# Kernel optimization log

Hardware: AMD Instinct MI355X
Metric: run time of the kernel (lower is better)

The kernel has to match this reference:

```python
import jax, jax.numpy as jnp
import numpy as np

B, L, H, NH, NE, M = 4, 1024, 768, 12, 42, 8
EMB = 768
OFFSET = 1  # bert cls offset


def setup_inputs() -> dict:
    key = jax.random.key(0)
    ks = jax.random.split(key, 6)
    seq = jax.random.normal(ks[0], (B, L, H), jnp.float32)
    attn = jax.random.uniform(ks[1], (B, NH, L, L), jnp.float32)
    attn = attn / attn.sum(-1, keepdims=True)  # row-stochastic like softmaxed attention probs
    W_head = jax.random.normal(ks[2], (2 * H, EMB), jnp.float32) * 0.02
    b_head = jnp.zeros((EMB,), jnp.float32)
    W_tail = jax.random.normal(ks[3], (2 * H, EMB), jnp.float32) * 0.02
    b_tail = jnp.zeros((EMB,), jnp.float32)
    # mention start positions (before +offset); keep start+offset < L
    mention_pos = jax.random.randint(ks[4], (B, NE, M), 0, L - OFFSET - 1)
    counts = jax.random.randint(ks[5], (B, NE), 1, M + 1)  # >=1 valid mention per entity
    mention_mask = jnp.arange(M)[None, None, :] < counts[:, :, None]
    return dict(sequence_output=seq, attention=attn, W_head=W_head, b_head=b_head,
                W_tail=W_tail, b_tail=b_tail, mention_pos=mention_pos,
                mention_mask=mention_mask)


def _get_hrt(seq, attn, mention_pos, mention_mask):
    # seq: [B,L,H]; attn: [B,NH,L,L]; mention_pos/mask: [B,NE,M]
    b_idx = jnp.arange(B)[:, None, None]
    pos = mention_pos + OFFSET                          # [B,NE,M]
    m_emb = seq[b_idx, pos]                             # [B,NE,M,H] mention embeddings
    att_t = jnp.transpose(attn, (0, 2, 1, 3))           # [B,L,NH,L]
    m_att = att_t[b_idx, pos]                           # [B,NE,M,NH,L] mention attentions
    mask = mention_mask
    neg_inf = jnp.finfo(seq.dtype).min
    # per-entity logsumexp pooling over mentions
    ent_emb = jax.nn.logsumexp(jnp.where(mask[..., None], m_emb, neg_inf), axis=2)
    has_m = mask.any(axis=2)
    ent_emb = jnp.where(has_m[..., None], ent_emb, 0.0)  # [B,NE,H]
    cnt = mask.sum(axis=2).astype(seq.dtype)
    ent_att = (m_att * mask[..., None, None].astype(seq.dtype)).sum(axis=2)
    ent_att = ent_att / jnp.maximum(cnt, 1.0)[..., None, None]  # [B,NE,NH,L] mean over mentions
    # all ordered (head, tail) pairs on the NE x NE grid
    hs = jnp.broadcast_to(ent_emb[:, :, None, :], (B, NE, NE, H))
    ts = jnp.broadcast_to(ent_emb[:, None, :, :], (B, NE, NE, H))
    # ht_att = relu(mean_h(h_att * t_att)), normalized over seq, then context = ht_att @ seq
    ht = jnp.einsum('bihl,bjhl->bijl', ent_att, ent_att) / NH  # [B,NE,NE,L]
    ht = jax.nn.relu(ht)
    ht = ht / (ht.sum(-1, keepdims=True) + 1e-10)
    rs = jnp.einsum('bijl,bld->bijd', ht, seq)                  # [B,NE,NE,H]
    return hs, rs, ts


def reference(sequence_output, attention, W_head, b_head, W_tail, b_tail, mention_pos, mention_mask):
    hs, rs, ts = _get_hrt(sequence_output, attention, mention_pos, mention_mask)
    h_out = jnp.tanh(jnp.concatenate([hs, rs], axis=-1) @ W_head + b_head)
    t_out = jnp.tanh(jnp.concatenate([ts, rs], axis=-1) @ W_tail + b_tail)
    return h_out, t_out
```

## Files before the change

### kernel.cpp

```cpp
#include <hip/hip_runtime.h>
#include <math.h>

typedef _Float16 f16;
typedef __attribute__((ext_vector_type(4))) _Float16 f16x4;
typedef __attribute__((ext_vector_type(8))) _Float16 f16x8;
typedef __attribute__((ext_vector_type(4))) float f32x4;

#define B_    4
#define L_    1024
#define H_    768
#define NH_   12
#define NE_   42
#define M_    8
#define E2_   1536
#define HTP_  1792
#define OUT_HALF 5419008LL

typedef __attribute__((address_space(1))) const unsigned char ga_t;
typedef __attribute__((address_space(3))) unsigned char la_t;
__device__ __forceinline__ void async16(const void* g, void* l) {
    __builtin_amdgcn_global_load_lds((ga_t*)g, (la_t*)l, 16, 0, 0);
}


__device__ void prep_body(int bid, char* smem,
                          const float* __restrict__ Wh, const float* __restrict__ Wt,
                          const float* __restrict__ bh, const float* __restrict__ bt,
                          f16* __restrict__ wtop, f16* __restrict__ wbot,
                          float* __restrict__ bcat) {
    float (*tile)[33] = (float(*)[33])smem;
    int tx = bid % 24, ty = (bid / 24) % 24, m = bid / 576;
    const float* src = (m & 1) ? Wt : Wh;
    int roff = (m & 2) ? H_ : 0;
    f16* dst = (m & 2) ? wbot : wtop;
    int coff = (m & 1) ? H_ : 0;
    int x = threadIdx.x & 31, y8 = threadIdx.x >> 5;
#pragma unroll
    for (int r = 0; r < 4; r++) {
        int h = ty*32 + y8 + r*8, c = tx*32 + x;
        tile[y8 + r*8][x] = src[(long long)(roff + h)*H_ + c];
    }
    __syncthreads();
#pragma unroll
    for (int r = 0; r < 4; r++) {
        int c2 = tx*32 + y8 + r*8, h2 = ty*32 + x;
        dst[(long long)(coff + c2)*H_ + h2] = (f16)tile[x][y8 + r*8];
    }
    if (bid == 0) {
        for (int idx = threadIdx.x; idx < E2_; idx += 256)
            bcat[idx] = (idx < H_) ? bh[idx] : bt[idx - H_];
    }
}

__device__ void seq16_body(int bid, const float* __restrict__ seq,
                           f16* __restrict__ seq16) {
    int idx = (bid*256 + threadIdx.x) * 4;
    f32x4 v = *(const f32x4*)(seq + idx);
    f16x4 o = {(f16)v[0], (f16)v[1], (f16)v[2], (f16)v[3]};
    *(f16x4*)(seq16 + idx) = o;
}

__device__ void ent_emb_body(int bid, const float* __restrict__ seq,
                             const int* __restrict__ mpos,
                             const int* __restrict__ mmask,
                             f16* __restrict__ ent) {
    int e = bid % NE_, b = bid / NE_;
    int tid = threadIdx.x;
    const int* mp = mpos  + (b*NE_ + e)*M_;
    const int* mk = mmask + (b*NE_ + e)*M_;
    int pos[M_], msk[M_];
#pragma unroll
    for (int m = 0; m < M_; m++) { msk[m] = mk[m]; pos[m] = mp[m] + 1; }
#pragma unroll
    for (int q = 0; q < 3; q++) {
        int h = tid + q*256;
        float mx = -1e30f, vals[M_];
#pragma unroll
        for (int m = 0; m < M_; m++) {
            vals[m] = 0.f;
            if (msk[m]) {
                float v = seq[((long long)b*L_ + pos[m])*H_ + h];
                vals[m] = v; mx = fmaxf(mx, v);
            }
        }
        float s = 0.f;
#pragma unroll
        for (int m = 0; m < M_; m++) if (msk[m]) s += expf(vals[m] - mx);
        float lse = (mx > -1e29f) ? mx + logf(s) : 0.f;
        ent[(b*NE_ + e)*H_ + h] = (f16)lse;
    }
}

__device__ void ent_att_body(int bid, const float* __restrict__ attn,
                             const int* __restrict__ mpos,
                             const int* __restrict__ mmask,
                             f16* __restrict__ eatt) {
    int nh = bid % NH_, e = (bid / NH_) % NE_, b = bid / (NH_*NE_);
    int tid = threadIdx.x;
    int l0 = tid * 4;
    const int* mp = mpos  + (b*NE_ + e)*M_;
    const int* mk = mmask + (b*NE_ + e)*M_;
    const float* abase = attn + (long long)(b*NH_ + nh) * L_ * L_;
    f32x4 acc = {0,0,0,0}; int cnt = 0;
#pragma unroll
    for (int m = 0; m < M_; m++) {
        if (mk[m]) {
            cnt++;
            const float* row = abase + (long long)(mp[m] + 1) * L_;
            acc += *(const f32x4*)(row + l0);
        }
    }
    float inv = 1.f / (float)(cnt > 0 ? cnt : 1);
    f16x4 o = {(f16)(acc[0]*inv), (f16)(acc[1]*inv), (f16)(acc[2]*inv), (f16)(acc[3]*inv)};
    *(f16x4*)(eatt + ((long long)(b*NE_ + e)*NH_ + nh)*L_ + l0) = o;
}

__device__ void ht_body(int bid, char* smem, const f16* __restrict__ eatt,
                        f16* __restrict__ HT) {
    int jg = bid % 6, i = (bid / 6) % NE_, b = bid / 252;
    int tid = threadIdx.x;
    f16* ei_s = (f16*)smem;
    float* red = (float*)(smem + NH_*L_*2);
    const f16* ei = eatt + (long long)(b*NE_ + i)*NH_*L_;
#pragma unroll
    for (int q = 0; q < 6; q++) {
        int off = (q*256 + tid)*8;
        *(f16x8*)(ei_s + off) = *(const f16x8*)(ei + off);
    }
    __syncthreads();
    int l0 = tid*4;
    int wave = tid >> 6, lane = tid & 63;
    for (int jj = 0; jj < 7; jj++) {
        int j = jg*7 + jj;
        const f16* ej = eatt + (long long)(b*NE_ + j)*NH_*L_;
        f32x4 acc = {0,0,0,0};
#pragma unroll
        for (int h = 0; h < NH_; h++) {
            f16x4 vi = *(const f16x4*)(ei_s + h*L_ + l0);
            f16x4 vj = *(const f16x4*)(ej   + h*L_ + l0);
#pragma unroll
            for (int r = 0; r < 4; r++) acc[r] += (float)vi[r] * (float)vj[r];
        }
        float v[4]; float s = 0.f;
#pragma unroll
        for (int r = 0; r < 4; r++) {
            float t = acc[r] * (1.f/12.f);
            t = t > 0.f ? t : 0.f;
            v[r] = t; s += t;
        }
#pragma unroll
        for (int m = 1; m < 64; m <<= 1) s += __shfl_xor(s, m, 64);
        if (lane == 0) red[wave] = s;
        __syncthreads();
        float S = red[0] + red[1] + red[2] + red[3];
        __syncthreads();
        float sc = 1.f / (S + 1e-10f);
        f16x4 o = {(f16)(v[0]*sc), (f16)(v[1]*sc), (f16)(v[2]*sc), (f16)(v[3]*sc)};
        *(f16x4*)(HT + ((long long)b*HTP_ + i*NE_ + j)*L_ + l0) = o;
    }
}

#define LDSS 40
__device__ void gemm_het_body(int bx, int by, char* smem,
                              const f16* __restrict__ A, const f16* __restrict__ BT,
                              float* __restrict__ het, const float* __restrict__ bcat) {
    const int M = 168, K = 768;
    f16* As = (f16*)smem;
    f16* Bs = (f16*)(smem + 64*LDSS*2);
    int bm = bx*64, bn = by*64;
    int tid = threadIdx.x;
    int wave = tid >> 6, lane = tid & 63;
    int wm = (wave >> 1)*32, wn = (wave & 1)*32;
    int lo4 = lane & 15, kq = (lane >> 4)*8;
    int srow = tid >> 2, scol = (tid & 3)*8;
    bool aval = (bm + srow) < M;
    const f16* aptr = A + (long long)(bm + srow)*K + scol;
    const f16* bptr = BT + (long long)(bn + srow)*K + scol;
    f32x4 acc[2][2] = {};
    for (int k0 = 0; k0 < K; k0 += 32) {
        uint4 zero = {0,0,0,0};
        uint4 av = aval ? *(const uint4*)(aptr + k0) : zero;
        uint4 bv = *(const uint4*)(bptr + k0);
        __syncthreads();
        *(uint4*)(As + srow*LDSS + scol) = av;
        *(uint4*)(Bs + srow*LDSS + scol) = bv;
        __syncthreads();
        f16x8 a0 = *(const f16x8*)(As + (wm +      lo4)*LDSS + kq);
        f16x8 a1 = *(const f16x8*)(As + (wm + 16 + lo4)*LDSS + kq);
        f16x8 b0 = *(const f16x8*)(Bs + (wn +      lo4)*LDSS + kq);
        f16x8 b1 = *(const f16x8*)(Bs + (wn + 16 + lo4)*LDSS + kq);
        acc[0][0] = __builtin_amdgcn_mfma_f32_16x16x32_f16(a0, b0, acc[0][0], 0,0,0);
        acc[0][1] = __builtin_amdgcn_mfma_f32_16x16x32_f16(a0, b1, acc[0][1], 0,0,0);
        acc[1][0] = __builtin_amdgcn_mfma_f32_16x16x32_f16(a1, b0, acc[1][0], 0,0,0);
        acc[1][1] = __builtin_amdgcn_mfma_f32_16x16x32_f16(a1, b1, acc[1][1], 0,0,0);
    }
    int rloc = (lane >> 4)*4;
#pragma unroll
    for (int sm = 0; sm < 2; sm++)
#pragma unroll
    for (int sn = 0; sn < 2; sn++) {
        f32x4 a = acc[sm][sn];
        int c  = bn + wn + sn*16 + lo4;
        int rb = bm + wm + sm*16 + rloc;
#pragma unroll
        for (int r = 0; r < 4; r++)
            if (rb + r < M) het[(rb + r)*E2_ + c] = a[r] + bcat[c];
    }
}

template<int MODE>
__device__ void gemm2_body(int bx, int by, int bz, char* smem,
                           const f16* __restrict__ A, const f16* __restrict__ BT, int K,
                           long long strideA, long long strideBT,
                           const float* __restrict__ het, float* __restrict__ outp,
                           f16* __restrict__ outp16) {
    f16* As = (f16*)smem;
    f16* Bs = (f16*)(smem + 8192);
    int bm = bx*128, bn = by*128;
    const f16* Ab = A + strideA*bz;
    const f16* Bb = BT + strideBT*bz;
    int tid = threadIdx.x, wave = tid >> 6, lane = tid & 63;
    int wm = (wave >> 1)*64, wn = (wave & 1)*64;
    int lo4 = lane & 15, kq = (lane >> 4)*8;
    int lrow = lane >> 2, lcol = (lane & 3)*8;
    const f16* ag = Ab + (long long)(bm + wave*32 + lrow)*K + lcol;
    const f16* bg = Bb + (long long)(bn + wave*32 + lrow)*K + lcol;
    f16* asl = As + wave*1024;
    f16* bsl = Bs + wave*1024;
    f32x4 acc[4][4] = {};
    for (int k0 = 0; k0 < K; k0 += 32) {
        async16(ag + k0,          asl);
        async16(ag + k0 + 16*K,   asl + 512);
        async16(bg + k0,          bsl);
        async16(bg + k0 + 16*K,   bsl + 512);
        __syncthreads();
        f16x8 af[4], bf[4];
#pragma unroll
        for (int s = 0; s < 4; s++) {
            af[s] = *(const f16x8*)(As + (wm + s*16 + lo4)*32 + kq);
            bf[s] = *(const f16x8*)(Bs + (wn + s*16 + lo4)*32 + kq);
        }
#pragma unroll
        for (int sm = 0; sm < 4; sm++)
#pragma unroll
        for (int sn = 0; sn < 4; sn++)
            acc[sm][sn] = __builtin_amdgcn_mfma_f32_16x16x32_f16(af[sm], bf[sn], acc[sm][sn], 0,0,0);
        __syncthreads();
    }
    int rloc = (lane >> 4)*4;
#pragma unroll
    for (int sm = 0; sm < 4; sm++)
#pragma unroll
    for (int sn = 0; sn < 4; sn++) {
        f32x4 a = acc[sm][sn];
        int c  = bn + wn + sn*16 + lo4;
        int rb = bm + wm + sm*16 + rloc;
        if constexpr (MODE == 1) {
            f16x4 o = {(f16)a[0], (f16)a[1], (f16)a[2], (f16)a[3]};
            *(f16x4*)(outp16 + (long long)bz*E2_*L_ + (long long)c*L_ + rb) = o;
        } else {
#pragma unroll
            for (int r = 0; r < 4; r++) {
                int row = rb + r;
                if (row < NE_*NE_) {
                    int i = row / NE_;
                    int j = row - i*NE_;
                    int sel = (c < H_) ? i : j;
                    float bias = het[(bz*NE_ + sel)*E2_ + c];
                    float v = tanhf(a[r] + bias);
                    long long o = (c < H_)
                        ? ((long long)((bz*NE_ + i)*NE_ + j))*H_ + c
                        : OUT_HALF + ((long long)((bz*NE_ + i)*NE_ + j))*H_ + (c - H_);
                    outp[o] = v;
                }
            }
        }
    }
}

__global__ __launch_bounds__(256) void k_L1(
        const float* __restrict__ seq, const float* __restrict__ attn,
        const float* __restrict__ Wh, const float* __restrict__ bh,
        const float* __restrict__ Wt, const float* __restrict__ bt,
        const int* __restrict__ mpos, const int* __restrict__ mmask,
        f16* __restrict__ wtop, f16* __restrict__ wbot, float* __restrict__ bcat,
        f16* __restrict__ seq16, f16* __restrict__ ent, f16* __restrict__ eatt) {
    __shared__ __align__(16) char smem[4224];
    int bid = blockIdx.x;
    if (bid < 2304)       prep_body(bid, smem, Wh, Wt, bh, bt, wtop, wbot, bcat);
    else if (bid < 5376)  seq16_body(bid - 2304, seq, seq16);
    else if (bid < 5544)  ent_emb_body(bid - 5376, seq, mpos, mmask, ent);
    else                  ent_att_body(bid - 5544, attn, mpos, mmask, eatt);
}

__global__ __launch_bounds__(256) void k_L2(
        const f16* __restrict__ seq16, const f16* __restrict__ wbot,
        const f16* __restrict__ ent, const f16* __restrict__ wtop,
        const float* __restrict__ bcat, const f16* __restrict__ eatt,
        f16* __restrict__ seqWT, float* __restrict__ het, f16* __restrict__ HT) {
    __shared__ __align__(16) char smem[24640];
    int bid = blockIdx.x;
    if (bid < 384) {
        int bx = bid & 7, by = (bid >> 3) % 12, bz = bid / 96;
        gemm2_body<1>(bx, by, bz, smem, seq16, wbot, 768,
                      (long long)L_*H_, 0, nullptr, nullptr, seqWT);
    } else if (bid < 1392) {
        ht_body(bid - 384, smem, eatt, HT);
    } else {
        int r = bid - 1392;
        gemm_het_body(r % 3, r / 3, smem, ent, wtop, het, bcat);
    }
}

__global__ __launch_bounds__(256) void k_L3(
        const f16* __restrict__ HT, const f16* __restrict__ seqWT,
        const float* __restrict__ het, float* __restrict__ outp) {
    __shared__ __align__(16) char smem[16384];
    gemm2_body<2>(blockIdx.x, blockIdx.y, blockIdx.z, smem, HT, seqWT, 1024,
                  (long long)HTP_*L_, (long long)E2_*L_, het, outp, nullptr);
}

extern "C" void kernel_launch(void* const* d_in, const int* in_sizes, int n_in,
                              void* d_out, int out_size, void* d_ws, size_t ws_size,
                              hipStream_t stream) {
    const float* seq  = (const float*)d_in[0];
    const float* attn = (const float*)d_in[1];
    const float* Wh   = (const float*)d_in[2];
    const float* bh   = (const float*)d_in[3];
    const float* Wt   = (const float*)d_in[4];
    const float* bt   = (const float*)d_in[5];
    const int* mpos   = (const int*)d_in[6];
    const int* mmask  = (const int*)d_in[7];
    float* out = (float*)d_out;
    char* ws = (char*)d_ws;
    f16*   ent   = (f16*)  (ws + 0);
    f16*   wtop  = (f16*)  (ws + 258048);
    f16*   wbot  = (f16*)  (ws + 2617344);
    float* bcat  = (float*)(ws + 4976640);
    float* het   = (float*)(ws + 4982784);
    f16*   eatt  = (f16*)  (ws + 6014976);
    f16*   seq16 = (f16*)  (ws + 10143744);
    f16*   HT    = (f16*)  (ws + 16435200);
    f16*   seqWT = (f16*)  (ws + 31115264);

    k_L1<<<7560, 256, 0, stream>>>(seq, attn, Wh, bh, Wt, bt, mpos, mmask,
                                   wtop, wbot, bcat, seq16, ent, eatt);
    k_L2<<<1464, 256, 0, stream>>>(seq16, wbot, ent, wtop, bcat, eatt,
                                   seqWT, het, HT);
    k_L3<<<dim3(14, 12, B_), 256, 0, stream>>>(HT, seqWT, het, out);
}
```

Baseline: 365.1 us.

## Fuse three launches into one persistent cooperative kernel with grid syncs

Result: slower. 558.1 us (+52.9%).

```diff
diff --git a/kernel.cpp b/kernel.cpp
--- a/kernel.cpp
+++ b/kernel.cpp
@@ -1,5 +1,8 @@
 #include <hip/hip_runtime.h>
+#include <hip/hip_cooperative_groups.h>
 #include <math.h>
+
+namespace cg = cooperative_groups;
 
 typedef _Float16 f16;
 typedef __attribute__((ext_vector_type(4))) _Float16 f16x4;
@@ -278,46 +281,46 @@
     }
 }
 
-__global__ __launch_bounds__(256) void k_L1(
+__global__ __launch_bounds__(256, 3) void k_all(
         const float* __restrict__ seq, const float* __restrict__ attn,
         const float* __restrict__ Wh, const float* __restrict__ bh,
         const float* __restrict__ Wt, const float* __restrict__ bt,
         const int* __restrict__ mpos, const int* __restrict__ mmask,
         f16* __restrict__ wtop, f16* __restrict__ wbot, float* __restrict__ bcat,
-        f16* __restrict__ seq16, f16* __restrict__ ent, f16* __restrict__ eatt) {
-    __shared__ __align__(16) char smem[4224];
-    int bid = blockIdx.x;
-    if (bid < 2304)       prep_body(bid, smem, Wh, Wt, bh, bt, wtop, wbot, bcat);
-    else if (bid < 5376)  seq16_body(bid - 2304, seq, seq16);
-    else if (bid < 5544)  ent_emb_body(bid - 5376, seq, mpos, mmask, ent);
-    else                  ent_att_body(bid - 5544, attn, mpos, mmask, eatt);
-}
-
-__global__ __launch_bounds__(256) void k_L2(
-        const f16* __restrict__ seq16, const f16* __restrict__ wbot,
-        const f16* __restrict__ ent, const f16* __restrict__ wtop,
-        const float* __restrict__ bcat, const f16* __restrict__ eatt,
-        f16* __restrict__ seqWT, float* __restrict__ het, f16* __restrict__ HT) {
+        f16* __restrict__ seq16, f16* __restrict__ ent, f16* __restrict__ eatt,
+        f16* __restrict__ seqWT, float* __restrict__ het, f16* __restrict__ HT,
+        float* __restrict__ outp) {
     __shared__ __align__(16) char smem[24640];
-    int bid = blockIdx.x;
-    if (bid < 384) {
-        int bx = bid & 7, by = (bid >> 3) % 12, bz = bid / 96;
-        gemm2_body<1>(bx, by, bz, smem, seq16, wbot, 768,
-                      (long long)L_*H_, 0, nullptr, nullptr, seqWT);
-    } else if (bid < 1392) {
-        ht_body(bid - 384, smem, eatt, HT);
-    } else {
-        int r = bid - 1392;
-        gemm_het_body(r % 3, r / 3, smem, ent, wtop, het, bcat);
-    }
-}
-
-__global__ __launch_bounds__(256) void k_L3(
-        const f16* __restrict__ HT, const f16* __restrict__ seqWT,
-        const float* __restrict__ het, float* __restrict__ outp) {
-    __shared__ __align__(16) char smem[16384];
-    gemm2_body<2>(blockIdx.x, blockIdx.y, blockIdx.z, smem, HT, seqWT, 1024,
-                  (long long)HTP_*L_, (long long)E2_*L_, het, outp, nullptr);
+    cg::grid_group grid = cg::this_grid();
+    int stride = gridDim.x;
+    for (int it = blockIdx.x; it < 7560; it += stride) {
+        if (it < 2016)       ent_att_body(it, attn, mpos, mmask, eatt);
+        else if (it < 2184)  ent_emb_body(it - 2016, seq, mpos, mmask, ent);
+        else if (it < 4488)  prep_body(it - 2184, smem, Wh, Wt, bh, bt, wtop, wbot, bcat);
+        else                 seq16_body(it - 4488, seq, seq16);
+        __syncthreads();
+    }
+    grid.sync();
+    for (int it = blockIdx.x; it < 1464; it += stride) {
+        if (it < 384) {
+            int bx = it & 7, by = (it >> 3) % 12, bz = it / 96;
+            gemm2_body<1>(bx, by, bz, smem, seq16, wbot, 768,
+                          (long long)L_*H_, 0, nullptr, nullptr, seqWT);
+        } else if (it < 1392) {
+            ht_body(it - 384, smem, eatt, HT);
+        } else {
+            int r = it - 1392;
+            gemm_het_body(r % 3, r / 3, smem, ent, wtop, het, bcat);
+        }
+        __syncthreads();
+    }
+    grid.sync();
+    for (int it = blockIdx.x; it < 672; it += stride) {
+        int bx = it % 14, by = (it / 14) % 12, bz = it / 168;
+        gemm2_body<2>(bx, by, bz, smem, HT, seqWT, 1024,
+                      (long long)HTP_*L_, (long long)E2_*L_, het, outp, nullptr);
+        __syncthreads();
+    }
 }
 
 extern "C" void kernel_launch(void* const* d_in, const int* in_sizes, int n_in,
@@ -343,9 +346,18 @@
     f16*   HT    = (f16*)  (ws + 16435200);
     f16*   seqWT = (f16*)  (ws + 31115264);
 
-    k_L1<<<7560, 256, 0, stream>>>(seq, attn, Wh, bh, Wt, bt, mpos, mmask,
-                                   wtop, wbot, bcat, seq16, ent, eatt);
-    k_L2<<<1464, 256, 0, stream>>>(seq16, wbot, ent, wtop, bcat, eatt,
-                                   seqWT, het, HT);
-    k_L3<<<dim3(14, 12, B_), 256, 0, stream>>>(HT, seqWT, het, out);
-}
+    int perCU = 0;
+    hipError_t e = hipOccupancyMaxActiveBlocksPerMultiprocessor(&perCU, (const void*)k_all, 256, 0);
+    if (e != hipSuccess || perCU < 1) perCU = 1;
+    int grid = perCU * 256;
+    if (grid > 768) grid = 768;
+
+    void* kargs[] = {
+        (void*)&seq, (void*)&attn, (void*)&Wh, (void*)&bh, (void*)&Wt, (void*)&bt,
+        (void*)&mpos, (void*)&mmask, (void*)&wtop, (void*)&wbot, (void*)&bcat,
+        (void*)&seq16, (void*)&ent, (void*)&eatt, (void*)&seqWT, (void*)&het,
+        (void*)&HT, (void*)&out
+    };
+    hipLaunchCooperativeKernel((const void*)k_all, dim3(grid), dim3(256),
+                               kargs, 0, stream);
+}
```
